# Optimization experiments

Measured on AMD Instinct MI355X. Metric: run time of the kernel, lower is better.

Reference implementation:

```python
import jax, jax.numpy as jnp
import numpy as np

N = 50000       # nodes
E = 800000      # edges (avg degree 16)
D = 64          # node_size
ES = 16         # edge_size = num_edge_types + 1
R = 3           # rounds_of_propagation
HG = 2 * D      # hG_size
MSG = 2 * D + ES  # 144


def setup_inputs() -> dict:
    key = jax.random.key(0)
    ks = jax.random.split(key, 20)
    s = 0.05
    return {
        "node_vectors": jax.random.normal(ks[0], (N, D), jnp.float32),
        "edge_vectors": jax.random.normal(ks[1], (E, ES), jnp.float32),
        "Wef": jax.random.normal(ks[2], (R, 2 * D, MSG), jnp.float32) * s,
        "bef": jnp.zeros((R, 2 * D), jnp.float32),
        "Wer": jax.random.normal(ks[3], (R, 2 * D, MSG), jnp.float32) * s,
        "ber": jnp.zeros((R, 2 * D), jnp.float32),
        "W_ih": jax.random.normal(ks[4], (R, 3 * D, 2 * D), jnp.float32) * s,
        "W_hh": jax.random.normal(ks[5], (R, 3 * D, D), jnp.float32) * s,
        "b_ih": jnp.zeros((R, 3 * D), jnp.float32),
        "b_hh": jnp.zeros((R, 3 * D), jnp.float32),
        "W_fm": jax.random.normal(ks[6], (HG, D), jnp.float32) * s,
        "b_fm": jnp.zeros((HG,), jnp.float32),
        "W_gm": jax.random.normal(ks[7], (HG, D), jnp.float32) * s,
        "b_gm": jnp.zeros((HG,), jnp.float32),
        "W_dec": jax.random.normal(ks[8], (1, HG + D), jnp.float32) * s,
        "b_dec": jnp.zeros((1,), jnp.float32),
        "u_indices": jax.random.randint(ks[9], (E,), 0, N, jnp.int32),
        "v_indices": jax.random.randint(ks[10], (E,), 0, N, jnp.int32),
        "target_idx": 0,
    }


def reference(node_vectors, edge_vectors, Wef, bef, Wer, ber, W_ih, W_hh,
              b_ih, b_hh, W_fm, b_fm, W_gm, b_gm, W_dec, b_dec,
              u_indices, v_indices, target_idx):
    n_nodes = node_vectors.shape[0]
    h = node_vectors
    for i in range(Wef.shape[0]):
        # gather endpoint features + edge features -> [E, MSG]
        raw = jnp.concatenate([h[u_indices], h[v_indices], edge_vectors], axis=1)
        msg_f = raw @ Wef[i].T + bef[i]   # [E, 2D]
        msg_r = raw @ Wer[i].T + ber[i]   # [E, 2D]
        # node.incoming -> edges where node is v; node.outgoing -> node is u
        agg = (jax.ops.segment_sum(msg_f, v_indices, num_segments=n_nodes)
               + jax.ops.segment_sum(msg_r, u_indices, num_segments=n_nodes))
        # torch GRUCell(agg, h)
        gi = agg @ W_ih[i].T + b_ih[i]
        gh = h @ W_hh[i].T + b_hh[i]
        i_r, i_z, i_n = jnp.split(gi, 3, axis=1)
        h_r, h_z, h_n = jnp.split(gh, 3, axis=1)
        r = jax.nn.sigmoid(i_r + h_r)
        z = jax.nn.sigmoid(i_z + h_z)
        n = jnp.tanh(i_n + r * h_n)
        h = (1.0 - z) * n + z * h
    # gated graph aggregation -> h_G [1, HG]
    h_G = jnp.sum((h @ W_fm.T + b_fm) * jax.nn.sigmoid(h @ W_gm.T + b_gm),
                  axis=0, keepdims=True)
    # add-edge decision logit
    feat = jnp.concatenate([h_G, h[target_idx][None, :]], axis=1)
    return feat @ W_dec.T + b_dec  # [1, 1]
```

## Files before the change

### kernel.cpp

```cpp
#include <hip/hip_runtime.h>
#include <math.h>

#define D64 64
#define ES16 16
#define NB5 256

typedef unsigned short u16;
typedef _Float16 half8 __attribute__((ext_vector_type(8)));
typedef __attribute__((ext_vector_type(4))) float f32x4;


__device__ __forceinline__ float sigf(float x){ return 1.0f/(1.0f + __expf(-x)); }
__device__ __forceinline__ float tanhfast(float x){ return 2.0f*sigf(2.0f*x) - 1.0f; }
__device__ __forceinline__ u16 f2h(float f){
  _Float16 h = (_Float16)f;
  u16 r; __builtin_memcpy(&r, &h, 2); return r;
}
__device__ __forceinline__ float h2f(u16 b){
  _Float16 h; __builtin_memcpy(&h, &b, 2); return (float)h;
}
__device__ __forceinline__ float2 up2(unsigned w){
  _Float16 lo, hi;
  u16 a = (u16)(w & 0xFFFF), b = (u16)(w >> 16);
  __builtin_memcpy(&lo, &a, 2); __builtin_memcpy(&hi, &b, 2);
  return make_float2((float)lo, (float)hi);
}

__global__ void k_count(const int* __restrict__ u, const int* __restrict__ v,
                        unsigned* __restrict__ cntp, int* __restrict__ rin,
                        int* __restrict__ rout, int N, int E){
  int e = blockIdx.x*256 + threadIdx.x;
  if(e < E){
    int kv = v[e];
    int ku = N + u[e];
    unsigned rv = atomicAdd(&cntp[kv >> 1], 1u << (16*(kv & 1)));
    unsigned ru = atomicAdd(&cntp[ku >> 1], 1u << (16*(ku & 1)));
    rin[e]  = (int)((rv >> (16*(kv & 1))) & 0xFFFFu);
    rout[e] = (int)((ru >> (16*(ku & 1))) & 0xFFFFu);
  }
}

__global__ void k_unpack(const unsigned* __restrict__ cntp, int* __restrict__ cnt, int M){
  int i = blockIdx.x*256 + threadIdx.x;
  if(i < M) cnt[i] = (int)((cntp[i >> 1] >> (16*(i & 1))) & 0xFFFFu);
}

__global__ void k_scan1(const int* __restrict__ cnt, int* __restrict__ part, int M){
  __shared__ int sm[256];
  int i = blockIdx.x*256 + threadIdx.x;
  sm[threadIdx.x] = (i < M) ? cnt[i] : 0;
  __syncthreads();
  for(int s = 128; s > 0; s >>= 1){
    if(threadIdx.x < s) sm[threadIdx.x] += sm[threadIdx.x + s];
    __syncthreads();
  }
  if(threadIdx.x == 0) part[blockIdx.x] = sm[0];
}

__global__ void k_scan2(int* __restrict__ part, int nb){
  __shared__ int sm[1024];
  int t = threadIdx.x;
  int orig = (t < nb) ? part[t] : 0;
  sm[t] = orig;
  __syncthreads();
  for(int off = 1; off < 1024; off <<= 1){
    int add = (t >= off) ? sm[t - off] : 0;
    __syncthreads();
    sm[t] += add;
    __syncthreads();
  }
  if(t < nb) part[t] = sm[t] - orig;
}

__global__ void k_scan3(int* __restrict__ cnt, const int* __restrict__ part,
                        int M, int total){
  __shared__ int sm[256];
  int t = threadIdx.x;
  int i = blockIdx.x*256 + t;
  int orig = (i < M) ? cnt[i] : 0;
  sm[t] = orig;
  __syncthreads();
  for(int off = 1; off < 256; off <<= 1){
    int add = (t >= off) ? sm[t - off] : 0;
    __syncthreads();
    sm[t] += add;
    __syncthreads();
  }
  if(i < M) cnt[i] = part[blockIdx.x] + sm[t] - orig;
  if(i == 0) cnt[M] = total;
}

__global__ void k_fill2(const int* __restrict__ u, const int* __restrict__ v,
                        const int* __restrict__ off, const int* __restrict__ rin,
                        const int* __restrict__ rout, int* __restrict__ rows,
                        int* __restrict__ srcs, int N, int E){
  int e = blockIdx.x*256 + threadIdx.x;
  if(e < E){
    int uu = u[e], vv = v[e];
    int p = off[vv] + rin[e];
    int q = off[N + uu] + rout[e];
    rows[p] = e; srcs[p] = uu;
    rows[q] = e; srcs[q] = vv;
  }
}

__global__ void k_cvt16(const float* __restrict__ src, u16* __restrict__ dst, int total){
  int i = blockIdx.x*256 + threadIdx.x;
  if(i < total) dst[i] = f2h(src[i]);
}

__global__ void k_einout(const float* __restrict__ ev, const int* __restrict__ off,
                         const int* __restrict__ rows,
                         float* __restrict__ Ein, float* __restrict__ Eout, int N){
  int n = (blockIdx.x*blockDim.x + threadIdx.x) >> 6;
  int lane = threadIdx.x & 63;
  if(n >= N) return;
  int t = lane & 15, s = lane >> 4;
  {
    float a0 = 0.f, a1 = 0.f;
    int p = off[n] + s, p1 = off[n+1];
    for(; p + 4 < p1; p += 8){
      a0 += ev[rows[p]*ES16 + t];
      a1 += ev[rows[p+4]*ES16 + t];
    }
    if(p < p1) a0 += ev[rows[p]*ES16 + t];
    float a = a0 + a1;
    a += __shfl_xor(a, 16, 64);
    a += __shfl_xor(a, 32, 64);
    if(lane < 16) Ein[n*ES16 + lane] = a;
  }
  {
    float b0 = 0.f, b1 = 0.f;
    int p = off[N+n] + s, p1 = off[N+n+1];
    for(; p + 4 < p1; p += 8){
      b0 += ev[rows[p]*ES16 + t];
      b1 += ev[rows[p+4]*ES16 + t];
    }
    if(p < p1) b0 += ev[rows[p]*ES16 + t];
    float b = b0 + b1;
    b += __shfl_xor(b, 16, 64);
    b += __shfl_xor(b, 32, 64);
    if(lane < 16) Eout[n*ES16 + lane] = b;
  }
}

__global__ void k_aggr(const u16* __restrict__ h16, const int* __restrict__ off,
                       const int* __restrict__ srcs,
                       u16* __restrict__ Sin16, u16* __restrict__ Sout16, int N){
  int n = (blockIdx.x*blockDim.x + threadIdx.x) >> 6;
  int lane = threadIdx.x & 63;
  if(n >= N) return;
  const int half = lane >> 5;
  const int fl   = lane & 31;
  const int gw   = half ? (N + n) : n;
  int p  = off[gw], p1 = off[gw+1];
  const unsigned* hsrc = (const unsigned*)h16;
  float sx0 = 0.f, sy0 = 0.f, sx1 = 0.f, sy1 = 0.f;
  for(; p + 16 <= p1; p += 16){
    int s[16]; unsigned w[16];
    #pragma unroll
    for(int j = 0; j < 16; ++j) s[j] = srcs[p + j];
    #pragma unroll
    for(int j = 0; j < 16; ++j) w[j] = hsrc[(size_t)s[j]*32 + fl];
    #pragma unroll
    for(int j = 0; j < 16; j += 4){
      float2 f0 = up2(w[j]), f1 = up2(w[j+1]), f2 = up2(w[j+2]), f3 = up2(w[j+3]);
      sx0 += f0.x + f1.x; sy0 += f0.y + f1.y;
      sx1 += f2.x + f3.x; sy1 += f2.y + f3.y;
    }
  }
  for(; p + 8 <= p1; p += 8){
    int s0 = srcs[p],   s1 = srcs[p+1], s2 = srcs[p+2], s3 = srcs[p+3];
    int s4 = srcs[p+4], s5 = srcs[p+5], s6 = srcs[p+6], s7 = srcs[p+7];
    unsigned w0 = hsrc[(size_t)s0*32 + fl];
    unsigned w1 = hsrc[(size_t)s1*32 + fl];
    unsigned w2 = hsrc[(size_t)s2*32 + fl];
    unsigned w3 = hsrc[(size_t)s3*32 + fl];
    unsigned w4 = hsrc[(size_t)s4*32 + fl];
    unsigned w5 = hsrc[(size_t)s5*32 + fl];
    unsigned w6 = hsrc[(size_t)s6*32 + fl];
    unsigned w7 = hsrc[(size_t)s7*32 + fl];
    float2 f0 = up2(w0), f1 = up2(w1), f2 = up2(w2), f3 = up2(w3);
    float2 f4 = up2(w4), f5 = up2(w5), f6 = up2(w6), f7 = up2(w7);
    sx0 += (f0.x + f1.x) + (f4.x + f5.x);
    sy0 += (f0.y + f1.y) + (f4.y + f5.y);
    sx1 += (f2.x + f3.x) + (f6.x + f7.x);
    sy1 += (f2.y + f3.y) + (f6.y + f7.y);
  }
  for(; p + 4 <= p1; p += 4){
    int s0 = srcs[p], s1 = srcs[p+1], s2 = srcs[p+2], s3 = srcs[p+3];
    unsigned w0 = hsrc[(size_t)s0*32 + fl];
    unsigned w1 = hsrc[(size_t)s1*32 + fl];
    unsigned w2 = hsrc[(size_t)s2*32 + fl];
    unsigned w3 = hsrc[(size_t)s3*32 + fl];
    float2 f0 = up2(w0), f1 = up2(w1), f2 = up2(w2), f3 = up2(w3);
    sx0 += f0.x + f1.x; sy0 += f0.y + f1.y;
    sx1 += f2.x + f3.x; sy1 += f2.y + f3.y;
  }
  for(; p < p1; ++p){
    float2 f0 = up2(hsrc[(size_t)srcs[p]*32 + fl]);
    sx0 += f0.x; sy0 += f0.y;
  }
  unsigned pw = (unsigned)f2h(sx0 + sx1) | ((unsigned)f2h(sy0 + sy1) << 16);
  unsigned* dst = half ? (unsigned*)Sout16 : (unsigned*)Sin16;
  dst[(size_t)n*32 + fl] = pw;
}

__global__ void k_pre(const float* __restrict__ Wef, const float* __restrict__ bef,
                      const float* __restrict__ Wer, const float* __restrict__ ber,
                      const float* __restrict__ Wih, const float* __restrict__ Whh,
                      const float* __restrict__ bih, const float* __restrict__ bhh,
                      const float* __restrict__ Wfm, const float* __restrict__ Wgm,
                      u16* __restrict__ bA, u16* __restrict__ bB,
                      u16* __restrict__ bC, int R){
  int b = blockIdx.x;
  int lane = threadIdx.x;
  u16 val8[8];
  u16* dst;
  if(b < R*80){
    int r = b / 80, t = b % 80;
    int nt = t / 10, kt = t % 10;
    int j = nt*16 + (lane & 15);
    int ks0 = kt*32 + (lane >> 4)*8;
    const float* wef = Wef + (size_t)r*128*144;
    const float* wer = Wer + (size_t)r*128*144;
    #pragma unroll
    for(int e = 0; e < 8; ++e){
      int ks = ks0 + e;
      float val;
      if(ks < 144)       val = wef[j*144 + ks];
      else if(ks == 144) val = bef[r*128 + j];
      else if(ks < 160)  val = 0.f;
      else if(ks < 304)  val = wer[j*144 + (ks - 160)];
      else if(ks == 304) val = ber[r*128 + j];
      else               val = 0.f;
      val8[e] = f2h(val);
    }
    dst = bA + ((size_t)b*64 + lane)*8;
  } else if(b < R*80 + R*96){
    int bb = b - R*80;
    int r = bb / 96, t = bb % 96;
    int nt = t / 8, kt = t % 8;
    int q = nt*16 + (lane & 15);
    int ks0 = kt*32 + (lane >> 4)*8;
    const float* wih = Wih + (size_t)r*192*128;
    const float* whh = Whh + (size_t)r*192*64;
    #pragma unroll
    for(int e = 0; e < 8; ++e){
      int ks = ks0 + e;
      float val;
      if(ks < 128)       val = wih[q*128 + ks];
      else if(ks == 128) val = bih[r*192 + q];
      else if(ks < 160)  val = 0.f;
      else if(ks < 224)  val = whh[q*64 + (ks - 160)];
      else if(ks == 224) val = bhh[r*192 + q];
      else               val = 0.f;
      val8[e] = f2h(val);
    }
    dst = bB + ((size_t)bb*64 + lane)*8;
  } else {
    int bb = b - R*80 - R*96;
    int nt = bb >> 2, kt = (bb >> 1) & 1, fg = bb & 1;
    int j = nt*16 + (lane & 15);
    int ks0 = kt*32 + (lane >> 4)*8;
    const float* W = fg ? Wgm : Wfm;
    #pragma unroll
    for(int e = 0; e < 8; ++e) val8[e] = f2h(W[j*64 + ks0 + e]);
    dst = bC + ((size_t)bb*64 + lane)*8;
  }
  #pragma unroll
  for(int e = 0; e < 8; ++e) dst[e] = val8[e];
}

__global__ __launch_bounds__(512) void k34_mfma(
    const u16* __restrict__ h16, const u16* __restrict__ Sin16,
    const u16* __restrict__ Sout16, const float* __restrict__ Ein,
    const float* __restrict__ Eout, const int* __restrict__ off,
    const u16* __restrict__ bA, const u16* __restrict__ bB,
    u16* __restrict__ h16next, int N){
  __shared__ u16 xA[64][328];
  __shared__ u16 x2[64][264];
  const int lane = threadIdx.x & 63;
  const int wv   = __builtin_amdgcn_readfirstlane(threadIdx.x >> 6);
  const int base = blockIdx.x * 64;

  for(int ii = 0; ii < 8; ++ii){
    int i = wv*8 + ii;
    int n = base + i; if(n >= N) n = N - 1;
    float fi = (float)(off[n+1] - off[n]);
    float fo = (float)(off[N+n+1] - off[N+n]);
    u16 hv16 = h16[(size_t)n*D64 + lane];
    float hv = h2f(hv16);
    xA[i][lane]        = Sin16[(size_t)n*D64 + lane];
    xA[i][64 + lane]   = f2h(fi*hv);
    xA[i][160 + lane]  = f2h(fo*hv);
    xA[i][224 + lane]  = Sout16[(size_t)n*D64 + lane];
    x2[i][160 + lane]  = hv16;
    if(lane < 16){
      xA[i][128 + lane] = f2h(Ein[(size_t)n*ES16 + lane]);
      xA[i][288 + lane] = f2h(Eout[(size_t)n*ES16 + lane]);
    }
    if(lane == 0){
      xA[i][144] = f2h(fi); xA[i][304] = f2h(fo);
      x2[i][128] = 0x3C00;  x2[i][224] = 0x3C00;
    }
    if(lane >= 1 && lane < 16){ xA[i][144 + lane] = 0; xA[i][304 + lane] = 0; }
    if(lane >= 1 && lane < 32){ x2[i][128 + lane] = 0; x2[i][224 + lane] = 0; }
  }
  __syncthreads();

  half8 bw[10];
  #pragma unroll
  for(int kt = 0; kt < 10; ++kt)
    bw[kt] = *(const half8*)(bA + ((size_t)(wv*10 + kt)*64 + lane)*8);

  f32x4 accA[4];
  const int arow = lane & 15;
  const int akof = (lane >> 4) * 8;
  #pragma unroll
  for(int m = 0; m < 4; ++m){
    f32x4 a = {0.f, 0.f, 0.f, 0.f};
    #pragma unroll
    for(int kt = 0; kt < 10; ++kt){
      half8 av = *(const half8*)&xA[m*16 + arow][kt*32 + akof];
      a = __builtin_amdgcn_mfma_f32_16x16x32_f16(av, bw[kt], a, 0, 0, 0);
    }
    accA[m] = a;
  }

  const int jb = wv * 16;
  #pragma unroll
  for(int m = 0; m < 4; ++m){
    #pragma unroll
    for(int reg = 0; reg < 4; ++reg){
      int nl = m*16 + (lane >> 4)*4 + reg;
      x2[nl][jb + (lane & 15)] = f2h(accA[m][reg]);
    }
  }
  __syncthreads();

  #pragma unroll
  for(int uu = 0; uu < 2; ++uu){
    const int unit = wv*2 + uu;
    const int mt  = unit >> 2;
    const int tri = unit & 3;
    f32x4 aR  = {0.f,0.f,0.f,0.f};
    f32x4 aZ  = {0.f,0.f,0.f,0.f};
    f32x4 aNi = {0.f,0.f,0.f,0.f};
    f32x4 aNh = {0.f,0.f,0.f,0.f};
    #pragma unroll
    for(int kt = 0; kt < 8; ++kt){
      half8 av = *(const half8*)&x2[mt*16 + arow][kt*32 + akof];
      half8 bR = *(const half8*)(bB + ((size_t)((tri    )*8 + kt)*64 + lane)*8);
      half8 bZ = *(const half8*)(bB + ((size_t)((tri + 4)*8 + kt)*64 + lane)*8);
      half8 bN = *(const half8*)(bB + ((size_t)((tri + 8)*8 + kt)*64 + lane)*8);
      aR = __builtin_amdgcn_mfma_f32_16x16x32_f16(av, bR, aR, 0, 0, 0);
      aZ = __builtin_amdgcn_mfma_f32_16x16x32_f16(av, bZ, aZ, 0, 0, 0);
      if(kt < 5) aNi = __builtin_amdgcn_mfma_f32_16x16x32_f16(av, bN, aNi, 0, 0, 0);
      else       aNh = __builtin_amdgcn_mfma_f32_16x16x32_f16(av, bN, aNh, 0, 0, 0);
    }
    const int q = tri*16 + (lane & 15);
    #pragma unroll
    for(int reg = 0; reg < 4; ++reg){
      int node = base + mt*16 + (lane >> 4)*4 + reg;
      float r  = sigf(aR[reg]);
      float z  = sigf(aZ[reg]);
      float nn = tanhfast(aNi[reg] + r*aNh[reg]);
      if(node < N){
        float hq = h2f(h16[(size_t)node*D64 + q]);
        h16next[(size_t)node*D64 + q] = f2h((1.f - z)*nn + z*hq);
      }
    }
  }
}

__global__ __launch_bounds__(512) void k5m(
    const u16* __restrict__ h16, const u16* __restrict__ bC,
    const float* __restrict__ bfm, const float* __restrict__ bgm,
    float* __restrict__ partials, int N, int nT){
  __shared__ u16 xh[64][72];
  const int lane = threadIdx.x & 63;
  const int wv   = __builtin_amdgcn_readfirstlane(threadIdx.x >> 6);
  const int arow = lane & 15;
  const int akof = (lane >> 4) * 8;
  half8 bF[2], bG[2];
  #pragma unroll
  for(int kt = 0; kt < 2; ++kt){
    bF[kt] = *(const half8*)(bC + ((size_t)(wv*4 + kt*2 + 0)*64 + lane)*8);
    bG[kt] = *(const half8*)(bC + ((size_t)(wv*4 + kt*2 + 1)*64 + lane)*8);
  }
  const float fb = bfm[wv*16 + arow];
  const float gb = bgm[wv*16 + arow];
  float acc = 0.f;
  for(int tile = blockIdx.x; tile < nT; tile += NB5){
    const int base = tile * 64;
    __syncthreads();
    for(int ii = 0; ii < 8; ++ii){
      int i = wv*8 + ii;
      int n = base + i;
      xh[i][lane] = (n < N) ? h16[(size_t)n*D64 + lane] : (u16)0;
    }
    __syncthreads();
    #pragma unroll
    for(int m = 0; m < 4; ++m){
      f32x4 F = {0.f,0.f,0.f,0.f};
      f32x4 G = {0.f,0.f,0.f,0.f};
      #pragma unroll
      for(int kt = 0; kt < 2; ++kt){
        half8 av = *(const half8*)&xh[m*16 + arow][kt*32 + akof];
        F = __builtin_amdgcn_mfma_f32_16x16x32_f16(av, bF[kt], F, 0, 0, 0);
        G = __builtin_amdgcn_mfma_f32_16x16x32_f16(av, bG[kt], G, 0, 0, 0);
      }
      #pragma unroll
      for(int reg = 0; reg < 4; ++reg){
        int node = base + m*16 + (lane >> 4)*4 + reg;
        if(node < N)
          acc += (F[reg] + fb) * sigf(G[reg] + gb);
      }
    }
  }
  acc += __shfl_xor(acc, 16, 64);
  acc += __shfl_xor(acc, 32, 64);
  if(lane < 16) partials[blockIdx.x*128 + wv*16 + lane] = acc;
}

__global__ void k6_dec(const float* __restrict__ partials, int nb,
                       const u16* __restrict__ h16,
                       const float* __restrict__ Wdec, const float* __restrict__ bdec,
                       const int* __restrict__ tgt, float* __restrict__ out){
  __shared__ float sm[256];
  int t = threadIdx.x;
  float v = 0.f;
  if(t < 128){
    float s0 = 0.f, s1 = 0.f, s2 = 0.f, s3 = 0.f;
    for(int b = 0; b + 4 <= nb; b += 4){
      s0 += partials[(b+0)*128 + t];
      s1 += partials[(b+1)*128 + t];
      s2 += partials[(b+2)*128 + t];
      s3 += partials[(b+3)*128 + t];
    }
    v = ((s0 + s1) + (s2 + s3)) * Wdec[t];
  } else if(t < 192){
    v = h2f(h16[(size_t)tgt[0]*D64 + (t - 128)]) * Wdec[t];
  }
  sm[t] = v;
  __syncthreads();
  for(int s = 128; s > 0; s >>= 1){
    if(t < s) sm[t] += sm[t + s];
    __syncthreads();
  }
  if(t == 0) out[0] = sm[0] + bdec[0];
}

extern "C" void kernel_launch(void* const* d_in, const int* in_sizes, int n_in,
                              void* d_out, int out_size, void* d_ws, size_t ws_size,
                              hipStream_t stream){
  const float* nodev = (const float*)d_in[0];
  const float* ev    = (const float*)d_in[1];
  const float* Wef   = (const float*)d_in[2];
  const float* bef   = (const float*)d_in[3];
  const float* Wer   = (const float*)d_in[4];
  const float* ber   = (const float*)d_in[5];
  const float* Wih   = (const float*)d_in[6];
  const float* Whh   = (const float*)d_in[7];
  const float* bih   = (const float*)d_in[8];
  const float* bhh   = (const float*)d_in[9];
  const float* Wfm   = (const float*)d_in[10];
  const float* bfm   = (const float*)d_in[11];
  const float* Wgm   = (const float*)d_in[12];
  const float* bgm   = (const float*)d_in[13];
  const float* Wdec  = (const float*)d_in[14];
  const float* bdec  = (const float*)d_in[15];
  const int* uidx    = (const int*)d_in[16];
  const int* vidx    = (const int*)d_in[17];
  const int* tgt     = (const int*)d_in[18];

  const int N = in_sizes[0] / 64;
  const int E = in_sizes[16];
  const int R = in_sizes[2] / (128*144);

  char* w = (char*)d_ws;
  auto alloc = [&](size_t bytes) -> void* {
    void* p = (void*)w;
    w += (bytes + 255) & ~(size_t)255;
    return p;
  };
  unsigned* cntp = (unsigned*)alloc(((size_t)N + 1) * 4);
  int* off       = (int*)alloc(((size_t)2*N + 1) * 4);
  int* rin       = (int*)alloc((size_t)E * 4);
  int* rout      = (int*)alloc((size_t)E * 4);
  int* rows      = (int*)alloc((size_t)2*E * 4);
  int* srcs      = (int*)alloc((size_t)2*E * 4);
  int* part      = (int*)alloc(4096 * 4);
  float* Ein     = (float*)alloc((size_t)N*16*4);
  float* Eout    = (float*)alloc((size_t)N*16*4);
  u16* Sin16     = (u16*)alloc((size_t)N*64*2);
  u16* Sout16    = (u16*)alloc((size_t)N*64*2);
  u16* g0        = (u16*)alloc((size_t)N*64*2);
  u16* gA        = (u16*)alloc((size_t)N*64*2);
  u16* gB        = (u16*)alloc((size_t)N*64*2);
  u16* bA        = (u16*)alloc((size_t)R*80*64*8*2);
  u16* bB        = (u16*)alloc((size_t)R*96*64*8*2);
  u16* bC        = (u16*)alloc((size_t)32*64*8*2);
  float* partial = (float*)alloc((size_t)NB5*128*4);

  hipMemsetAsync(cntp, 0, ((size_t)N+1)*4, stream);

  int eb = (E + 255)/256;
  k_count<<<eb, 256, 0, stream>>>(uidx, vidx, cntp, rin, rout, N, E);
  int M = 2*N;
  int nb = (M + 255)/256;
  k_unpack<<<nb, 256, 0, stream>>>(cntp, off, M);
  k_scan1<<<nb, 256, 0, stream>>>(off, part, M);
  k_scan2<<<1, 1024, 0, stream>>>(part, nb);
  k_scan3<<<nb, 256, 0, stream>>>(off, part, M, 2*E);
  k_fill2<<<eb, 256, 0, stream>>>(uidx, vidx, off, rin, rout, rows, srcs, N, E);
  int wb = (N + 3)/4;
  k_einout<<<wb, 256, 0, stream>>>(ev, off, rows, Ein, Eout, N);
  k_cvt16<<<(N*64 + 255)/256, 256, 0, stream>>>(nodev, g0, N*64);

  k_pre<<<R*80 + R*96 + 32, 64, 0, stream>>>(Wef, bef, Wer, ber, Wih, Whh,
                                             bih, bhh, Wfm, Wgm, bA, bB, bC, R);

  int nT = (N + 63)/64;
  const u16* g16cur = g0;
  u16* gbufs[2] = {gA, gB};
  for(int r = 0; r < R; ++r){
    k_aggr<<<wb, 256, 0, stream>>>(g16cur, off, srcs, Sin16, Sout16, N);
    u16* gn = gbufs[r & 1];
    k34_mfma<<<nT, 512, 0, stream>>>(g16cur, Sin16, Sout16, Ein, Eout, off,
                                     bA + (size_t)r*80*64*8,
                                     bB + (size_t)r*96*64*8,
                                     gn, N);
    g16cur = gn;
  }
  k5m<<<NB5, 512, 0, stream>>>(g16cur, bC, bfm, bgm, partial, N, nT);
  k6_dec<<<1, 256, 0, stream>>>(partial, NB5, g16cur, Wdec, bdec, tgt, (float*)d_out);
}
```

Measured before the change: 422.4 us.

## Fuse neighbor aggregation into GRU MFMA kernel and use plain int degree counters

The per-round gather-sum over incoming and outgoing neighbors now runs inside the MFMA GRU kernel and writes straight into its shared-memory input tile. This removes the separate aggregation launch and the global round trip through the Sin16/Sout16 buffers. Degree counting also switches from packed 16-bit atomics to 32-bit atomics on the offset array, which drops the unpack kernel. The trade-off is that the gather now runs with the MFMA kernel's occupancy (512 threads plus large LDS), which may hide the random-access latency less well than the standalone kernel did.

Result: slower. 480.7 us (+13.8%).

```diff
diff --git a/kernel.cpp b/kernel.cpp
--- a/kernel.cpp
+++ b/kernel.cpp
@@ -27,22 +27,13 @@
 }
 
 __global__ void k_count(const int* __restrict__ u, const int* __restrict__ v,
-                        unsigned* __restrict__ cntp, int* __restrict__ rin,
+                        int* __restrict__ cnt, int* __restrict__ rin,
                         int* __restrict__ rout, int N, int E){
   int e = blockIdx.x*256 + threadIdx.x;
   if(e < E){
-    int kv = v[e];
-    int ku = N + u[e];
-    unsigned rv = atomicAdd(&cntp[kv >> 1], 1u << (16*(kv & 1)));
-    unsigned ru = atomicAdd(&cntp[ku >> 1], 1u << (16*(ku & 1)));
-    rin[e]  = (int)((rv >> (16*(kv & 1))) & 0xFFFFu);
-    rout[e] = (int)((ru >> (16*(ku & 1))) & 0xFFFFu);
-  }
-}
-
-__global__ void k_unpack(const unsigned* __restrict__ cntp, int* __restrict__ cnt, int M){
-  int i = blockIdx.x*256 + threadIdx.x;
-  if(i < M) cnt[i] = (int)((cntp[i >> 1] >> (16*(i & 1))) & 0xFFFFu);
+    rin[e]  = atomicAdd(&cnt[v[e]], 1);
+    rout[e] = atomicAdd(&cnt[N + u[e]], 1);
+  }
 }
 
 __global__ void k_scan1(const int* __restrict__ cnt, int* __restrict__ part, int M){
@@ -142,68 +133,6 @@
     b += __shfl_xor(b, 32, 64);
     if(lane < 16) Eout[n*ES16 + lane] = b;
   }
-}
-
-__global__ void k_aggr(const u16* __restrict__ h16, const int* __restrict__ off,
-                       const int* __restrict__ srcs,
-                       u16* __restrict__ Sin16, u16* __restrict__ Sout16, int N){
-  int n = (blockIdx.x*blockDim.x + threadIdx.x) >> 6;
-  int lane = threadIdx.x & 63;
-  if(n >= N) return;
-  const int half = lane >> 5;
-  const int fl   = lane & 31;
-  const int gw   = half ? (N + n) : n;
-  int p  = off[gw], p1 = off[gw+1];
-  const unsigned* hsrc = (const unsigned*)h16;
-  float sx0 = 0.f, sy0 = 0.f, sx1 = 0.f, sy1 = 0.f;
-  for(; p + 16 <= p1; p += 16){
-    int s[16]; unsigned w[16];
-    #pragma unroll
-    for(int j = 0; j < 16; ++j) s[j] = srcs[p + j];
-    #pragma unroll
-    for(int j = 0; j < 16; ++j) w[j] = hsrc[(size_t)s[j]*32 + fl];
-    #pragma unroll
-    for(int j = 0; j < 16; j += 4){
-      float2 f0 = up2(w[j]), f1 = up2(w[j+1]), f2 = up2(w[j+2]), f3 = up2(w[j+3]);
-      sx0 += f0.x + f1.x; sy0 += f0.y + f1.y;
-      sx1 += f2.x + f3.x; sy1 += f2.y + f3.y;
-    }
-  }
-  for(; p + 8 <= p1; p += 8){
-    int s0 = srcs[p],   s1 = srcs[p+1], s2 = srcs[p+2], s3 = srcs[p+3];
-    int s4 = srcs[p+4], s5 = srcs[p+5], s6 = srcs[p+6], s7 = srcs[p+7];
-    unsigned w0 = hsrc[(size_t)s0*32 + fl];
-    unsigned w1 = hsrc[(size_t)s1*32 + fl];
-    unsigned w2 = hsrc[(size_t)s2*32 + fl];
-    unsigned w3 = hsrc[(size_t)s3*32 + fl];
-    unsigned w4 = hsrc[(size_t)s4*32 + fl];
-    unsigned w5 = hsrc[(size_t)s5*32 + fl];
-    unsigned w6 = hsrc[(size_t)s6*32 + fl];
-    unsigned w7 = hsrc[(size_t)s7*32 + fl];
-    float2 f0 = up2(w0), f1 = up2(w1), f2 = up2(w2), f3 = up2(w3);
-    float2 f4 = up2(w4), f5 = up2(w5), f6 = up2(w6), f7 = up2(w7);
-    sx0 += (f0.x + f1.x) + (f4.x + f5.x);
-    sy0 += (f0.y + f1.y) + (f4.y + f5.y);
-    sx1 += (f2.x + f3.x) + (f6.x + f7.x);
-    sy1 += (f2.y + f3.y) + (f6.y + f7.y);
-  }
-  for(; p + 4 <= p1; p += 4){
-    int s0 = srcs[p], s1 = srcs[p+1], s2 = srcs[p+2], s3 = srcs[p+3];
-    unsigned w0 = hsrc[(size_t)s0*32 + fl];
-    unsigned w1 = hsrc[(size_t)s1*32 + fl];
-    unsigned w2 = hsrc[(size_t)s2*32 + fl];
-    unsigned w3 = hsrc[(size_t)s3*32 + fl];
-    float2 f0 = up2(w0), f1 = up2(w1), f2 = up2(w2), f3 = up2(w3);
-    sx0 += f0.x + f1.x; sy0 += f0.y + f1.y;
-    sx1 += f2.x + f3.x; sy1 += f2.y + f3.y;
-  }
-  for(; p < p1; ++p){
-    float2 f0 = up2(hsrc[(size_t)srcs[p]*32 + fl]);
-    sx0 += f0.x; sy0 += f0.y;
-  }
-  unsigned pw = (unsigned)f2h(sx0 + sx1) | ((unsigned)f2h(sy0 + sy1) << 16);
-  unsigned* dst = half ? (unsigned*)Sout16 : (unsigned*)Sin16;
-  dst[(size_t)n*32 + fl] = pw;
 }
 
 __global__ void k_pre(const float* __restrict__ Wef, const float* __restrict__ bef,
@@ -272,10 +201,10 @@
   for(int e = 0; e < 8; ++e) dst[e] = val8[e];
 }
 
-__global__ __launch_bounds__(512) void k34_mfma(
-    const u16* __restrict__ h16, const u16* __restrict__ Sin16,
-    const u16* __restrict__ Sout16, const float* __restrict__ Ein,
+__global__ __launch_bounds__(512) void k34f(
+    const u16* __restrict__ h16, const float* __restrict__ Ein,
     const float* __restrict__ Eout, const int* __restrict__ off,
+    const int* __restrict__ srcs,
     const u16* __restrict__ bA, const u16* __restrict__ bB,
     u16* __restrict__ h16next, int N){
   __shared__ u16 xA[64][328];
@@ -283,6 +212,67 @@
   const int lane = threadIdx.x & 63;
   const int wv   = __builtin_amdgcn_readfirstlane(threadIdx.x >> 6);
   const int base = blockIdx.x * 64;
+  const unsigned* hsrc = (const unsigned*)h16;
+
+  {
+    const int half = lane >> 5;
+    const int fl   = lane & 31;
+    const int roff = (half ? 224 : 0) + fl*2;
+    for(int ii = 0; ii < 8; ++ii){
+      int i = wv*8 + ii;
+      int n = base + i; if(n >= N) n = N - 1;
+      const int gw = half ? (N + n) : n;
+      int p = off[gw], p1 = off[gw+1];
+      float sx0 = 0.f, sy0 = 0.f, sx1 = 0.f, sy1 = 0.f;
+      for(; p + 16 <= p1; p += 16){
+        int s[16]; unsigned w[16];
+        #pragma unroll
+        for(int j = 0; j < 16; ++j) s[j] = srcs[p + j];
+        #pragma unroll
+        for(int j = 0; j < 16; ++j) w[j] = hsrc[(size_t)s[j]*32 + fl];
+        #pragma unroll
+        for(int j = 0; j < 16; j += 4){
+          float2 f0 = up2(w[j]), f1 = up2(w[j+1]), f2 = up2(w[j+2]), f3 = up2(w[j+3]);
+          sx0 += f0.x + f1.x; sy0 += f0.y + f1.y;
+          sx1 += f2.x + f3.x; sy1 += f2.y + f3.y;
+        }
+      }
+      for(; p + 8 <= p1; p += 8){
+        int s0 = srcs[p],   s1 = srcs[p+1], s2 = srcs[p+2], s3 = srcs[p+3];
+        int s4 = srcs[p+4], s5 = srcs[p+5], s6 = srcs[p+6], s7 = srcs[p+7];
+        unsigned w0 = hsrc[(size_t)s0*32 + fl];
+        unsigned w1 = hsrc[(size_t)s1*32 + fl];
+        unsigned w2 = hsrc[(size_t)s2*32 + fl];
+        unsigned w3 = hsrc[(size_t)s3*32 + fl];
+        unsigned w4 = hsrc[(size_t)s4*32 + fl];
+        unsigned w5 = hsrc[(size_t)s5*32 + fl];
+        unsigned w6 = hsrc[(size_t)s6*32 + fl];
+        unsigned w7 = hsrc[(size_t)s7*32 + fl];
+        float2 f0 = up2(w0), f1 = up2(w1), f2 = up2(w2), f3 = up2(w3);
+        float2 f4 = up2(w4), f5 = up2(w5), f6 = up2(w6), f7 = up2(w7);
+        sx0 += (f0.x + f1.x) + (f4.x + f5.x);
+        sy0 += (f0.y + f1.y) + (f4.y + f5.y);
+        sx1 += (f2.x + f3.x) + (f6.x + f7.x);
+        sy1 += (f2.y + f3.y) + (f6.y + f7.y);
+      }
+      for(; p + 4 <= p1; p += 4){
+        int s0 = srcs[p], s1 = srcs[p+1], s2 = srcs[p+2], s3 = srcs[p+3];
+        unsigned w0 = hsrc[(size_t)s0*32 + fl];
+        unsigned w1 = hsrc[(size_t)s1*32 + fl];
+        unsigned w2 = hsrc[(size_t)s2*32 + fl];
+        unsigned w3 = hsrc[(size_t)s3*32 + fl];
+        float2 f0 = up2(w0), f1 = up2(w1), f2 = up2(w2), f3 = up2(w3);
+        sx0 += f0.x + f1.x; sy0 += f0.y + f1.y;
+        sx1 += f2.x + f3.x; sy1 += f2.y + f3.y;
+      }
+      for(; p < p1; ++p){
+        float2 f0 = up2(hsrc[(size_t)srcs[p]*32 + fl]);
+        sx0 += f0.x; sy0 += f0.y;
+      }
+      unsigned pw = (unsigned)f2h(sx0 + sx1) | ((unsigned)f2h(sy0 + sy1) << 16);
+      *(unsigned*)&xA[i][roff] = pw;
+    }
+  }
 
   for(int ii = 0; ii < 8; ++ii){
     int i = wv*8 + ii;
@@ -291,10 +281,8 @@
     float fo = (float)(off[N+n+1] - off[N+n]);
     u16 hv16 = h16[(size_t)n*D64 + lane];
     float hv = h2f(hv16);
-    xA[i][lane]        = Sin16[(size_t)n*D64 + lane];
     xA[i][64 + lane]   = f2h(fi*hv);
     xA[i][160 + lane]  = f2h(fo*hv);
-    xA[i][224 + lane]  = Sout16[(size_t)n*D64 + lane];
     x2[i][160 + lane]  = hv16;
     if(lane < 16){
       xA[i][128 + lane] = f2h(Ein[(size_t)n*ES16 + lane]);
@@ -485,7 +473,6 @@
     w += (bytes + 255) & ~(size_t)255;
     return p;
   };
-  unsigned* cntp = (unsigned*)alloc(((size_t)N + 1) * 4);
   int* off       = (int*)alloc(((size_t)2*N + 1) * 4);
   int* rin       = (int*)alloc((size_t)E * 4);
   int* rout      = (int*)alloc((size_t)E * 4);
@@ -494,8 +481,6 @@
   int* part      = (int*)alloc(4096 * 4);
   float* Ein     = (float*)alloc((size_t)N*16*4);
   float* Eout    = (float*)alloc((size_t)N*16*4);
-  u16* Sin16     = (u16*)alloc((size_t)N*64*2);
-  u16* Sout16    = (u16*)alloc((size_t)N*64*2);
   u16* g0        = (u16*)alloc((size_t)N*64*2);
   u16* gA        = (u16*)alloc((size_t)N*64*2);
   u16* gB        = (u16*)alloc((size_t)N*64*2);
@@ -504,13 +489,12 @@
   u16* bC        = (u16*)alloc((size_t)32*64*8*2);
   float* partial = (float*)alloc((size_t)NB5*128*4);
 
-  hipMemsetAsync(cntp, 0, ((size_t)N+1)*4, stream);
+  hipMemsetAsync(off, 0, ((size_t)2*N+1)*4, stream);
 
   int eb = (E + 255)/256;
-  k_count<<<eb, 256, 0, stream>>>(uidx, vidx, cntp, rin, rout, N, E);
+  k_count<<<eb, 256, 0, stream>>>(uidx, vidx, off, rin, rout, N, E);
   int M = 2*N;
   int nb = (M + 255)/256;
-  k_unpack<<<nb, 256, 0, stream>>>(cntp, off, M);
   k_scan1<<<nb, 256, 0, stream>>>(off, part, M);
   k_scan2<<<1, 1024, 0, stream>>>(part, nb);
   k_scan3<<<nb, 256, 0, stream>>>(off, part, M, 2*E);
@@ -526,12 +510,11 @@
   const u16* g16cur = g0;
   u16* gbufs[2] = {gA, gB};
   for(int r = 0; r < R; ++r){
-    k_aggr<<<wb, 256, 0, stream>>>(g16cur, off, srcs, Sin16, Sout16, N);
     u16* gn = gbufs[r & 1];
-    k34_mfma<<<nT, 512, 0, stream>>>(g16cur, Sin16, Sout16, Ein, Eout, off,
-                                     bA + (size_t)r*80*64*8,
-                                     bB + (size_t)r*96*64*8,
-                                     gn, N);
+    k34f<<<nT, 512, 0, stream>>>(g16cur, Ein, Eout, off, srcs,
+                                 bA + (size_t)r*80*64*8,
+                                 bB + (size_t)r*96*64*8,
+                                 gn, N);
     g16cur = gn;
   }
   k5m<<<NB5, 512, 0, stream>>>(g16cur, bC, bfm, bgm, partial, N, nT);
```
